# Kernel optimization log

Hardware: AMD Instinct MI355X
Metric: run time of the kernel (lower is better)

The kernel has to match this reference:

```python
import jax, jax.numpy as jnp
import numpy as np

NH, HD = 8, 32  # num_heads, head_dim (visual_dim=256)
BASE = 10000.0

def _inv_freq(dim):
    return 1.0 / (BASE ** (jnp.arange(0, dim, 2, dtype=jnp.float32) / dim))

def rotate_half(x):
    x1, x2 = jnp.split(x, 2, axis=-1)
    return jnp.concatenate([-x2, x1], axis=-1)

def rope3d_freqs(D, H, W, head_dim):
    zd = head_dim // 3; yd = head_dim // 3; xd = head_dim - zd - yd
    fz = jnp.arange(D, dtype=jnp.float32)[:, None] * _inv_freq(zd)  # [D, zd/2]
    fy = jnp.arange(H, dtype=jnp.float32)[:, None] * _inv_freq(yd)
    fx = jnp.arange(W, dtype=jnp.float32)[:, None] * _inv_freq(xd)
    ez = jnp.broadcast_to(jnp.concatenate([fz, fz], -1)[:, None, None, :], (D, H, W, zd))
    ey = jnp.broadcast_to(jnp.concatenate([fy, fy], -1)[None, :, None, :], (D, H, W, yd))
    ex = jnp.broadcast_to(jnp.concatenate([fx, fx], -1)[None, None, :, :], (D, H, W, xd))
    return jnp.concatenate([ez, ey, ex], axis=-1)  # [D,H,W,head_dim]

def apply_rope(q, freqs):
    return q * jnp.cos(freqs) + rotate_half(q) * jnp.sin(freqs)

def setup_inputs() -> dict:
    key = jax.random.key(0)
    ks = jax.random.split(key, 16)
    B, C, D, H, W, S, TD = 2, 256, 32, 32, 32, 256, 512
    s = 0.02
    return {
        'fused_visual': jax.random.normal(ks[0], (B, C, D, H, W), jnp.float32),
        'text_embedding': jax.random.normal(ks[1], (B, S, TD), jnp.float32),
        'q_w': jax.random.normal(ks[2], (C, C), jnp.float32) * s,
        'q_b': jnp.zeros((C,), jnp.float32),
        'k_w': jax.random.normal(ks[3], (TD, C), jnp.float32) * s,
        'k_b': jnp.zeros((C,), jnp.float32),
        'v_w': jax.random.normal(ks[4], (TD, C), jnp.float32) * s,
        'v_b': jnp.zeros((C,), jnp.float32),
        'o_w': jax.random.normal(ks[5], (C, C), jnp.float32) * s,
        'o_b': jnp.zeros((C,), jnp.float32),
        'm1_w': jax.random.normal(ks[6], (TD, TD // 2), jnp.float32) * s,
        'm1_b': jnp.zeros((TD // 2,), jnp.float32),
        'm2_w': jax.random.normal(ks[7], (TD // 2, NH * HD), jnp.float32) * s,
        'm2_b': jnp.zeros((NH * HD,), jnp.float32),
    }

def reference(fused_visual, text_embedding, q_w, q_b, k_w, k_b, v_w, v_b,
              o_w, o_b, m1_w, m1_b, m2_w, m2_b):
    B, C, D, H, W = fused_visual.shape
    S = text_embedding.shape[1]
    scale = HD ** -0.5
    fv = jnp.transpose(fused_visual, (0, 2, 3, 4, 1))  # [B,D,H,W,C]
    q = (fv @ q_w + q_b).reshape(B, D, H, W, NH, HD)
    q = jnp.transpose(q, (0, 4, 1, 2, 3, 5))            # [B,nH,D,H,W,hd]
    k = jnp.transpose((text_embedding @ k_w + k_b).reshape(B, S, NH, HD), (0, 2, 1, 3))
    v = jnp.transpose((text_embedding @ v_w + v_b).reshape(B, S, NH, HD), (0, 2, 1, 3))
    freqs = rope3d_freqs(D, H, W, HD)[None, None]       # [1,1,D,H,W,hd]
    q_rot = apply_rope(q, freqs)
    # learned text phase (exact GELU as in torch default)
    h = jax.nn.gelu(text_embedding @ m1_w + m1_b, approximate=False)
    phase = jnp.transpose((h @ m2_w + m2_b).reshape(B, S, NH, HD), (0, 2, 1, 3))
    k_rot = apply_rope(k, phase)
    q_flat = q_rot.reshape(B, NH, D * H * W, HD)
    attn = jax.nn.softmax(jnp.einsum('bhnd,bhsd->bhns', q_flat, k_rot) * scale, axis=-1)
    out = jnp.einsum('bhns,bhsd->bhnd', attn, v)        # [B,nH,N,hd]
    out = out.reshape(B, NH, D, H, W, HD)
    out = jnp.transpose(out, (0, 2, 3, 4, 1, 5)).reshape(B, D, H, W, C)
    out = out @ o_w + o_b
    return jnp.transpose(out, (0, 4, 1, 2, 3))          # [B,C,D,H,W]
```

## Files before the change

### kernel.cpp

```cpp
#include <hip/hip_runtime.h>
#include <hip/hip_bf16.h>

#define NHD 8
#define HD  32
#define C_  256
#define TD_ 512
#define S_  256
#define N_  32768
#define B_  2

typedef short bf16x8 __attribute__((ext_vector_type(8)));
typedef short bf16x4 __attribute__((ext_vector_type(4)));
typedef float f32x4  __attribute__((ext_vector_type(4)));

#define MFMA16(a,b,c) __builtin_amdgcn_mfma_f32_16x16x32_bf16(a,b,c,0,0,0)

__device__ __forceinline__ short f2bf(float f){
    __hip_bfloat16 h = __float2bfloat16(f);
    return *reinterpret_cast<short*>(&h);
}

typedef __attribute__((address_space(3))) unsigned int lds_u32;
typedef const __attribute__((address_space(1))) unsigned int glb_u32;

__device__ __forceinline__ void async_cp16(const void* g, void* l){
    __builtin_amdgcn_global_load_lds(
        (glb_u32*)(unsigned long long)g,
        (lds_u32*)(unsigned int)(unsigned long long)l,
        16, 0, 0);
}

__device__ __forceinline__ void stage_tile(const short* __restrict__ g, short* l, int tid){
    const int wvb = tid & 192;
#pragma unroll
    for (int r = 0; r < 4; ++r)
        async_cp16(g + (r * 256 + tid) * 8, l + (r * 256 + wvb) * 8);
}

#define TS_LD(Ka, Va, Ma, Ta, j0) \
    _Pragma("unroll") for (int i = 0; i < 16; ++i) { \
        Ka[i] = kp[(j0 + i) * C_]; Va[i] = vp[(j0 + i) * C_]; \
        Ma[i] = mp[(j0 + i) * C_]; Ta[i] = t_s[(j0) + i]; }
#define TS_FM(Ka, Va, Ma, Ta) \
    _Pragma("unroll") for (int i = 0; i < 16; ++i) { \
        kv += Ta[i] * Ka[i]; vv += Ta[i] * Va[i]; hv += Ta[i] * Ma[i]; }
#define M2_LD(Ha, Ga, j0) \
    _Pragma("unroll") for (int i = 0; i < 16; ++i) { \
        Ha[i] = h_s[(j0) + i]; Ga[i] = m2p[(j0 + i) * C_]; }
#define M2_FM(Ha, Ga) \
    _Pragma("unroll") for (int i = 0; i < 16; ++i) { ph += Ha[i] * Ga[i]; }

__global__ __launch_bounds__(256, 2) void text_stage(
    const float* __restrict__ text,
    const float* __restrict__ k_w, const float* __restrict__ k_b,
    const float* __restrict__ v_w, const float* __restrict__ v_b,
    const float* __restrict__ m1_w, const float* __restrict__ m1_b,
    const float* __restrict__ m2_w, const float* __restrict__ m2_b,
    const float* __restrict__ qw, const float* __restrict__ ow,
    short* __restrict__ kf, short* __restrict__ vf,
    short* __restrict__ wqf, short* __restrict__ wof)
{
    const int tid = threadIdx.x;

    if (blockIdx.x >= 512) {
        int gid = (blockIdx.x - 512) * 256 + tid;
        int m = gid >> 13;
        int rest = gid & 8191;
        const float* src = m ? ow : qw;
        short* dst = m ? wof : wqf;
        int lane = rest & 63;
        int l15 = lane & 15, qd = lane >> 4;
        int cbase, co;
        if (m == 0) { int nt = rest >> 9, cc = (rest >> 6) & 7; cbase = cc * 32 + qd * 8; co = nt * 16 + l15; }
        else        { int hm = rest >> 6; cbase = (hm >> 4) * 32 + qd * 8; co = (hm & 15) * 16 + l15; }
        bf16x8 r;
#pragma unroll
        for (int j = 0; j < 8; ++j) r[j] = f2bf(src[(size_t)(cbase + j) * 256 + co]);
        *(bf16x8*)&dst[(size_t)rest * 8] = r;
        return;
    }

    __shared__ float t_s[TD_];
    __shared__ float h_s[C_];
    __shared__ float k_s[C_];
    const int token = blockIdx.x;

    float2 tt = *(const float2*)&text[(size_t)token * TD_ + tid * 2];
    t_s[tid * 2] = tt.x; t_s[tid * 2 + 1] = tt.y;
    __syncthreads();

    float kv = k_b[tid], vv = v_b[tid], hv = m1_b[tid];
    const float* kp = k_w + tid;
    const float* vp = v_w + tid;
    const float* mp = m1_w + tid;

    {
        float Ka[16], Va[16], Ma[16], Ta[16];
        float Kb[16], Vb[16], Mb[16], Tb[16];
        TS_LD(Ka, Va, Ma, Ta, 0);
#pragma unroll 1
        for (int jb = 0; jb < TD_; jb += 32) {
            TS_LD(Kb, Vb, Mb, Tb, jb + 16);
            TS_FM(Ka, Va, Ma, Ta);
            if (jb + 32 < TD_) { TS_LD(Ka, Va, Ma, Ta, jb + 32); }
            TS_FM(Kb, Vb, Mb, Tb);
        }
    }

    float hg = 0.5f * hv * (1.0f + erff(hv * 0.70710678118654752f));
    h_s[tid] = hg;
    k_s[tid] = kv;
    __syncthreads();

    float ph = m2_b[tid];
    const float* m2p = m2_w + tid;
    {
        float Ha[16], Ga[16], Hb[16], Gb[16];
        M2_LD(Ha, Ga, 0);
#pragma unroll 1
        for (int jb = 0; jb < C_; jb += 32) {
            M2_LD(Hb, Gb, jb + 16);
            M2_FM(Ha, Ga);
            if (jb + 32 < C_) { M2_LD(Ha, Ga, jb + 32); }
            M2_FM(Hb, Gb);
        }
    }

    const int t = tid & (HD - 1);
    const int nh = tid >> 5;
    const int b = token >> 8, s = token & (S_ - 1);
    const int bh = b * NHD + nh;
    float partner = (t < 16) ? -k_s[tid + 16] : k_s[tid - 16];
    float kr = kv * cosf(ph) + partner * sinf(ph);
    kf[(((size_t)bh * 16 + (s >> 4)) * 64 + (t >> 3) * 16 + (s & 15)) * 8 + (t & 7)] = f2bf(kr);
    vf[((((size_t)bh * 8 + (s >> 5)) * 2 + (t >> 4)) * 64 + ((s >> 3) & 3) * 16 + (t & 15)) * 8 + (s & 7)] = f2bf(vv);
}

__device__ __forceinline__ float freq3d(int t, int n){
    int d = n >> 10, h = (n >> 5) & 31, w = n & 31;
    float pos, ex;
    if (t < 10)      { pos = (float)d; ex = (float)(2 * (t % 5)) * 0.1f; }
    else if (t < 20) { pos = (float)h; ex = (float)(2 * ((t - 10) % 5)) * 0.1f; }
    else             { pos = (float)w; ex = (float)(2 * ((t - 20) % 6)) * (1.0f / 12.0f); }
    return pos * expf(-ex * 9.210340371976184f);
}

__global__ __launch_bounds__(256, 4) void fused_visual(
    const float* __restrict__ fv, const short* __restrict__ wqf,
    const float* __restrict__ q_b, const short* __restrict__ kf,
    const short* __restrict__ vf, const short* __restrict__ wof,
    const float* __restrict__ o_b, float* __restrict__ out)
{
    __shared__ __align__(16) short Stg[16384];
    __shared__ __align__(16) short Pb[4 * 16 * 64];
    const int tid = threadIdx.x;
    const int lane = tid & 63;
    const int l15 = tid & 15, qd = (tid >> 4) & 3, wv = tid >> 6;
    const int n0 = blockIdx.x * 64;
    const int b = blockIdx.y;
    const f32x4 z4 = {0.f, 0.f, 0.f, 0.f};
    const float scale = 0.17677669529663687f;

    short* slot0 = Stg;
    short* slot1 = Stg + 8192;

    bf16x8 af[8];
    const float* Tsf = (const float*)Stg;
#pragma unroll
    for (int ch = 0; ch < 2; ++ch) {
#pragma unroll
        for (int r = 0; r < 8; ++r) {
            int slot = r * 256 + tid;
            int c_loc = slot >> 4;
            int u = (slot & 15) ^ (c_loc & 15);
            async_cp16(fv + (size_t)(b * C_ + ch * 128 + c_loc) * N_ + n0 + u * 4,
                       Stg + (r * 256 + (tid & 192)) * 8);
        }
        __syncthreads();
#pragma unroll
        for (int cc2 = 0; cc2 < 4; ++cc2) {
            bf16x8 a;
#pragma unroll
            for (int j = 0; j < 8; ++j) {
                int c_loc = cc2 * 32 + qd * 8 + j;
                int u = (wv * 4 + (l15 >> 2)) ^ (c_loc & 15);
                float x = Tsf[c_loc * 64 + u * 4 + (l15 & 3)];
                a[j] = f2bf(x);
            }
            af[ch * 4 + cc2] = a;
        }
        __syncthreads();
    }

    f32x4 acc[16];
#pragma unroll
    for (int i = 0; i < 16; ++i) acc[i] = z4;

    stage_tile(wqf, slot0, tid);

#pragma unroll
    for (int ntp = 0; ntp < 8; ++ntp) {
        __syncthreads();
        if (ntp < 7) stage_tile(wqf + (ntp + 1) * 8192, (ntp & 1) ? slot0 : slot1, tid);
        const short* sb = (ntp & 1) ? slot1 : slot0;
#pragma unroll
        for (int cc = 0; cc < 8; ++cc)
#pragma unroll
            for (int ntl = 0; ntl < 2; ++ntl) {
                bf16x8 bq = *(const bf16x8*)&sb[((ntl * 8 + cc) * 64 + lane) * 8];
                acc[ntp * 2 + ntl] = MFMA16(af[cc], bq, acc[ntp * 2 + ntl]);
            }
    }
    __syncthreads();

    short* Qsc = Stg + wv * 4096;
#pragma unroll
    for (int r = 0; r < 4; ++r) {
        int lr = qd * 4 + r;
        int n = n0 + wv * 16 + lr;
        int key = lr & 7;
        float f1 = freq3d(l15, n), f2 = freq3d(l15 + 16, n);
        float c1 = cosf(f1), s1 = sinf(f1), c2 = cosf(f2), s2 = sinf(f2);
#pragma unroll
        for (int hh = 0; hh < 8; ++hh) {
            float x1 = acc[2 * hh][r]     + q_b[hh * 32 + l15];
            float x2 = acc[2 * hh + 1][r] + q_b[hh * 32 + 16 + l15];
            int cb1 = (hh * 4 + (l15 >> 3)) ^ key;
            int cb2 = (hh * 4 + 2 + (l15 >> 3)) ^ key;
            Qsc[lr * 256 + cb1 * 8 + (l15 & 7)] = f2bf((x1 * c1 - x2 * s1) * scale);
            Qsc[lr * 256 + cb2 * 8 + (l15 & 7)] = f2bf((x2 * c2 + x1 * s2) * scale);
        }
    }
    bf16x8 aqh[8];
#pragma unroll
    for (int h = 0; h < 8; ++h)
        aqh[h] = *(const bf16x8*)&Qsc[l15 * 256 + ((h * 4 + qd) ^ (l15 & 7)) * 8];

    __syncthreads();
    stage_tile(kf + (size_t)(b * NHD) * 8192, slot0, tid);

    f32x4 acc_co[16];
#pragma unroll
    for (int i = 0; i < 16; ++i) acc_co[i] = z4;
    short* Pw = Pb + wv * 16 * 64;
    short* Ow = Pw;

#pragma unroll
    for (int h = 0; h < 8; ++h) {
        const int bh = b * NHD + h;
        __syncthreads();
        stage_tile(wof + (size_t)h * 8192, slot1, tid);

        const short* vbase = vf + (size_t)bh * 8192;

        float tsum[4] = {0.f, 0.f, 0.f, 0.f};
        f32x4 o0 = z4, o1 = z4;

#pragma unroll
        for (int qt = 0; qt < 4; ++qt) {
            f32x4 sc[4];
#pragma unroll
            for (int s4 = 0; s4 < 4; ++s4) {
                bf16x8 bk = *(const bf16x8*)&slot0[(qt * 4 + s4) * 512 + lane * 8];
                sc[s4] = MFMA16(aqh[h], bk, z4);
            }
#pragma unroll
            for (int s4 = 0; s4 < 4; ++s4)
#pragma unroll
                for (int r = 0; r < 4; ++r) {
                    sc[s4][r] = __expf(sc[s4][r]);
                    tsum[r] += sc[s4][r];
                }
#pragma unroll
            for (int s4 = 0; s4 < 4; ++s4)
#pragma unroll
                for (int r = 0; r < 4; ++r) {
                    int row = qd * 4 + r;
                    Pw[row * 64 + ((s4 * 2 + (l15 >> 3)) ^ (row & 7)) * 8 + (l15 & 7)] = f2bf(sc[s4][r]);
                }
#pragma unroll
            for (int ktl = 0; ktl < 2; ++ktl) {
                bf16x8 pa = *(const bf16x8*)&Pw[l15 * 64 + ((ktl * 4 + qd) ^ (l15 & 7)) * 8];
                int kt = qt * 2 + ktl;
                bf16x8 v0 = *(const bf16x8*)&vbase[(kt * 2 + 0) * 512 + lane * 8];
                bf16x8 v1 = *(const bf16x8*)&vbase[(kt * 2 + 1) * 512 + lane * 8];
                o0 = MFMA16(pa, v0, o0);
                o1 = MFMA16(pa, v1, o1);
            }
        }
        float il[4];
#pragma unroll
        for (int r = 0; r < 4; ++r) {
            float t = tsum[r];
            t += __shfl_xor(t, 1); t += __shfl_xor(t, 2);
            t += __shfl_xor(t, 4); t += __shfl_xor(t, 8);
            il[r] = 1.f / t;
        }
#pragma unroll
        for (int r = 0; r < 4; ++r) {
            int row = qd * 4 + r;
            int key = row & 3;
            Ow[row * 32 + (((l15 >> 3) ^ key) & 3) * 8 + (l15 & 7)]       = f2bf(o0[r] * il[r]);
            Ow[row * 32 + (((2 + (l15 >> 3)) ^ key) & 3) * 8 + (l15 & 7)] = f2bf(o1[r] * il[r]);
        }

        __syncthreads();
        if (h < 7)
            stage_tile(kf + (size_t)(bh + 1) * 8192, slot0, tid);

        bf16x8 bo = *(const bf16x8*)&Ow[l15 * 32 + ((qd ^ (l15 & 3)) & 3) * 8];
#pragma unroll
        for (int mt = 0; mt < 16; ++mt) {
            bf16x8 ao = *(const bf16x8*)&slot1[mt * 512 + lane * 8];
            acc_co[mt] = MFMA16(ao, bo, acc_co[mt]);
        }
    }

#pragma unroll
    for (int mt = 0; mt < 16; ++mt)
#pragma unroll
        for (int r = 0; r < 4; ++r) {
            int co = mt * 16 + qd * 4 + r;
            out[(size_t)(b * C_ + co) * N_ + n0 + wv * 16 + l15] = acc_co[mt][r] + o_b[co];
        }
}

extern "C" void kernel_launch(void* const* d_in, const int* in_sizes, int n_in,
                              void* d_out, int out_size, void* d_ws, size_t ws_size,
                              hipStream_t stream) {
    (void)in_sizes; (void)n_in; (void)out_size; (void)ws_size;
    const float* fv   = (const float*)d_in[0];
    const float* text = (const float*)d_in[1];
    const float* q_w  = (const float*)d_in[2];
    const float* q_b  = (const float*)d_in[3];
    const float* k_w  = (const float*)d_in[4];
    const float* k_b  = (const float*)d_in[5];
    const float* v_w  = (const float*)d_in[6];
    const float* v_b  = (const float*)d_in[7];
    const float* o_w  = (const float*)d_in[8];
    const float* o_b  = (const float*)d_in[9];
    const float* m1_w = (const float*)d_in[10];
    const float* m1_b = (const float*)d_in[11];
    const float* m2_w = (const float*)d_in[12];
    const float* m2_b = (const float*)d_in[13];
    float* out = (float*)d_out;

    short* wsS  = (short*)d_ws;
    short* kf   = wsS;
    short* vf   = wsS + 131072;
    short* wqf  = wsS + 262144;
    short* wof  = wsS + 327680;

    hipLaunchKernelGGL(text_stage, dim3(576), dim3(256), 0, stream,
                       text, k_w, k_b, v_w, v_b, m1_w, m1_b, m2_w, m2_b,
                       q_w, o_w, kf, vf, wqf, wof);
    hipLaunchKernelGGL(fused_visual, dim3(512, 2), dim3(256), 0, stream,
                       fv, wqf, q_b, kf, vf, wof, o_b, out);
}
```

Baseline: 270.0 us.

## Split text stage into two batched-token kernels and load visual input directly

The per-token text projection kernel becomes two kernels. text1 handles 4 tokens per block for the K/V/M1 projections plus GELU, and text2 handles 8 tokens per block for the M2 phase projection and the K RoPE. Weight loads are reused across several tokens, which cuts redundant global weight traffic, at the cost of an extra launch and fp32 intermediates round-tripping through the workspace. In the visual kernel, the input tile is now read directly from global memory into registers instead of staged through LDS, and the first Wq tile stage is issued earlier so it overlaps that load.

```diff
diff --git a/kernel.cpp b/kernel.cpp
--- a/kernel.cpp
+++ b/kernel.cpp
@@ -37,33 +37,25 @@
         async_cp16(g + (r * 256 + tid) * 8, l + (r * 256 + wvb) * 8);
 }
 
-#define TS_LD(Ka, Va, Ma, Ta, j0) \
-    _Pragma("unroll") for (int i = 0; i < 16; ++i) { \
-        Ka[i] = kp[(j0 + i) * C_]; Va[i] = vp[(j0 + i) * C_]; \
-        Ma[i] = mp[(j0 + i) * C_]; Ta[i] = t_s[(j0) + i]; }
-#define TS_FM(Ka, Va, Ma, Ta) \
-    _Pragma("unroll") for (int i = 0; i < 16; ++i) { \
-        kv += Ta[i] * Ka[i]; vv += Ta[i] * Va[i]; hv += Ta[i] * Ma[i]; }
-#define M2_LD(Ha, Ga, j0) \
-    _Pragma("unroll") for (int i = 0; i < 16; ++i) { \
-        Ha[i] = h_s[(j0) + i]; Ga[i] = m2p[(j0 + i) * C_]; }
-#define M2_FM(Ha, Ga) \
-    _Pragma("unroll") for (int i = 0; i < 16; ++i) { ph += Ha[i] * Ga[i]; }
-
-__global__ __launch_bounds__(256, 2) void text_stage(
+#define T1_LD(K,V,M,j0) _Pragma("unroll") for(int i=0;i<8;++i){ \
+    K[i]=kp[(j0+i)*C_]; V[i]=vp[(j0+i)*C_]; M[i]=mp[(j0+i)*C_]; }
+#define T1_FM(K,V,M,j0) _Pragma("unroll") for(int i=0;i<8;++i){ \
+    _Pragma("unroll") for(int m=0;m<4;++m){ float tv=t_s[m*TD_+j0+i]; \
+        accK[m]+=tv*K[i]; accV[m]+=tv*V[i]; accH[m]+=tv*M[i]; } }
+
+__global__ __launch_bounds__(256) void text1(
     const float* __restrict__ text,
     const float* __restrict__ k_w, const float* __restrict__ k_b,
     const float* __restrict__ v_w, const float* __restrict__ v_b,
     const float* __restrict__ m1_w, const float* __restrict__ m1_b,
-    const float* __restrict__ m2_w, const float* __restrict__ m2_b,
     const float* __restrict__ qw, const float* __restrict__ ow,
-    short* __restrict__ kf, short* __restrict__ vf,
+    float* __restrict__ kraw, float* __restrict__ vraw, float* __restrict__ hgb,
     short* __restrict__ wqf, short* __restrict__ wof)
 {
     const int tid = threadIdx.x;
 
-    if (blockIdx.x >= 512) {
-        int gid = (blockIdx.x - 512) * 256 + tid;
+    if (blockIdx.x >= 128) {
+        int gid = (blockIdx.x - 128) * 256 + tid;
         int m = gid >> 13;
         int rest = gid & 8191;
         const float* src = m ? ow : qw;
@@ -80,60 +72,95 @@
         return;
     }
 
-    __shared__ float t_s[TD_];
-    __shared__ float h_s[C_];
-    __shared__ float k_s[C_];
-    const int token = blockIdx.x;
-
-    float2 tt = *(const float2*)&text[(size_t)token * TD_ + tid * 2];
-    t_s[tid * 2] = tt.x; t_s[tid * 2 + 1] = tt.y;
+    __shared__ float t_s[4 * TD_];
+    const int tok0 = blockIdx.x * 4;
+#pragma unroll
+    for (int i = 0; i < 2; ++i) {
+        int idx = i * 256 + tid;
+        *(float4*)&t_s[idx * 4] = *(const float4*)&text[(size_t)tok0 * TD_ + idx * 4];
+    }
     __syncthreads();
 
-    float kv = k_b[tid], vv = v_b[tid], hv = m1_b[tid];
+    float accK[4], accV[4], accH[4];
+#pragma unroll
+    for (int m = 0; m < 4; ++m) { accK[m] = k_b[tid]; accV[m] = v_b[tid]; accH[m] = m1_b[tid]; }
     const float* kp = k_w + tid;
     const float* vp = v_w + tid;
     const float* mp = m1_w + tid;
 
     {
-        float Ka[16], Va[16], Ma[16], Ta[16];
-        float Kb[16], Vb[16], Mb[16], Tb[16];
-        TS_LD(Ka, Va, Ma, Ta, 0);
+        float ka[8], va[8], ma[8], kb2[8], vb2[8], mb2[8];
+        T1_LD(ka, va, ma, 0);
 #pragma unroll 1
-        for (int jb = 0; jb < TD_; jb += 32) {
-            TS_LD(Kb, Vb, Mb, Tb, jb + 16);
-            TS_FM(Ka, Va, Ma, Ta);
-            if (jb + 32 < TD_) { TS_LD(Ka, Va, Ma, Ta, jb + 32); }
-            TS_FM(Kb, Vb, Mb, Tb);
-        }
-    }
-
-    float hg = 0.5f * hv * (1.0f + erff(hv * 0.70710678118654752f));
-    h_s[tid] = hg;
-    k_s[tid] = kv;
+        for (int j0 = 0; j0 < TD_; j0 += 16) {
+            T1_LD(kb2, vb2, mb2, j0 + 8);
+            T1_FM(ka, va, ma, j0);
+            if (j0 + 16 < TD_) { T1_LD(ka, va, ma, j0 + 16); }
+            T1_FM(kb2, vb2, mb2, j0 + 8);
+        }
+    }
+
+#pragma unroll
+    for (int m = 0; m < 4; ++m) {
+        kraw[(size_t)(tok0 + m) * C_ + tid] = accK[m];
+        vraw[(size_t)(tok0 + m) * C_ + tid] = accV[m];
+        float hv = accH[m];
+        hgb[(size_t)(tok0 + m) * C_ + tid] = 0.5f * hv * (1.0f + erff(hv * 0.70710678118654752f));
+    }
+}
+
+#define T2_LD(G, j0) _Pragma("unroll") for (int i = 0; i < 8; ++i) G[i] = m2p[(j0 + i) * C_];
+#define T2_FM(G, j0) _Pragma("unroll") for (int i = 0; i < 8; ++i) { \
+    _Pragma("unroll") for (int m = 0; m < 8; ++m) accP[m] += h_s[m * C_ + j0 + i] * G[i]; }
+
+__global__ __launch_bounds__(256) void text2(
+    const float* __restrict__ m2_w, const float* __restrict__ m2_b,
+    const float* __restrict__ kraw, const float* __restrict__ vraw,
+    const float* __restrict__ hgb,
+    short* __restrict__ kf, short* __restrict__ vf)
+{
+    __shared__ float h_s[8 * C_];
+    const int tid = threadIdx.x;
+    const int tok0 = blockIdx.x * 8;
+#pragma unroll
+    for (int i = 0; i < 2; ++i) {
+        int idx = i * 256 + tid;
+        *(float4*)&h_s[idx * 4] = *(const float4*)&hgb[(size_t)tok0 * C_ + idx * 4];
+    }
     __syncthreads();
 
-    float ph = m2_b[tid];
+    float accP[8];
+#pragma unroll
+    for (int m = 0; m < 8; ++m) accP[m] = m2_b[tid];
     const float* m2p = m2_w + tid;
     {
-        float Ha[16], Ga[16], Hb[16], Gb[16];
-        M2_LD(Ha, Ga, 0);
+        float ga[8], gb2[8];
+        T2_LD(ga, 0);
 #pragma unroll 1
-        for (int jb = 0; jb < C_; jb += 32) {
-            M2_LD(Hb, Gb, jb + 16);
-            M2_FM(Ha, Ga);
-            if (jb + 32 < C_) { M2_LD(Ha, Ga, jb + 32); }
-            M2_FM(Hb, Gb);
+        for (int j0 = 0; j0 < C_; j0 += 16) {
+            T2_LD(gb2, j0 + 8);
+            T2_FM(ga, j0);
+            if (j0 + 16 < C_) { T2_LD(ga, j0 + 16); }
+            T2_FM(gb2, j0 + 8);
         }
     }
 
     const int t = tid & (HD - 1);
     const int nh = tid >> 5;
-    const int b = token >> 8, s = token & (S_ - 1);
-    const int bh = b * NHD + nh;
-    float partner = (t < 16) ? -k_s[tid + 16] : k_s[tid - 16];
-    float kr = kv * cosf(ph) + partner * sinf(ph);
-    kf[(((size_t)bh * 16 + (s >> 4)) * 64 + (t >> 3) * 16 + (s & 15)) * 8 + (t & 7)] = f2bf(kr);
-    vf[((((size_t)bh * 8 + (s >> 5)) * 2 + (t >> 4)) * 64 + ((s >> 3) & 3) * 16 + (t & 15)) * 8 + (s & 7)] = f2bf(vv);
+#pragma unroll
+    for (int m = 0; m < 8; ++m) {
+        int token = tok0 + m;
+        int b = token >> 8, s = token & (S_ - 1);
+        int bh = b * NHD + nh;
+        float kv = kraw[(size_t)token * C_ + tid];
+        float vv = vraw[(size_t)token * C_ + tid];
+        float partner = (t < 16) ? -kraw[(size_t)token * C_ + tid + 16]
+                                 :  kraw[(size_t)token * C_ + tid - 16];
+        float ph = accP[m];
+        float kr = kv * cosf(ph) + partner * sinf(ph);
+        kf[(((size_t)bh * 16 + (s >> 4)) * 64 + (t >> 3) * 16 + (s & 15)) * 8 + (t & 7)] = f2bf(kr);
+        vf[((((size_t)bh * 8 + (s >> 5)) * 2 + (t >> 4)) * 64 + ((s >> 3) & 3) * 16 + (t & 15)) * 8 + (s & 7)] = f2bf(vv);
+    }
 }
 
 __device__ __forceinline__ float freq3d(int t, int n){
@@ -164,39 +191,25 @@
     short* slot0 = Stg;
     short* slot1 = Stg + 8192;
 
+    stage_tile(wqf, slot0, tid);
+
     bf16x8 af[8];
-    const float* Tsf = (const float*)Stg;
-#pragma unroll
-    for (int ch = 0; ch < 2; ++ch) {
-#pragma unroll
-        for (int r = 0; r < 8; ++r) {
-            int slot = r * 256 + tid;
-            int c_loc = slot >> 4;
-            int u = (slot & 15) ^ (c_loc & 15);
-            async_cp16(fv + (size_t)(b * C_ + ch * 128 + c_loc) * N_ + n0 + u * 4,
-                       Stg + (r * 256 + (tid & 192)) * 8);
-        }
-        __syncthreads();
-#pragma unroll
-        for (int cc2 = 0; cc2 < 4; ++cc2) {
-            bf16x8 a;
-#pragma unroll
-            for (int j = 0; j < 8; ++j) {
-                int c_loc = cc2 * 32 + qd * 8 + j;
-                int u = (wv * 4 + (l15 >> 2)) ^ (c_loc & 15);
-                float x = Tsf[c_loc * 64 + u * 4 + (l15 & 3)];
-                a[j] = f2bf(x);
-            }
-            af[ch * 4 + cc2] = a;
-        }
-        __syncthreads();
+    {
+        const float* fbase = fv + ((size_t)b * C_) * N_ + n0 + wv * 16 + l15;
+#pragma unroll
+        for (int cc = 0; cc < 8; ++cc) {
+            float tmp[8];
+#pragma unroll
+            for (int j = 0; j < 8; ++j)
+                tmp[j] = fbase[(size_t)(cc * 32 + qd * 8 + j) * N_];
+#pragma unroll
+            for (int j = 0; j < 8; ++j) af[cc][j] = f2bf(tmp[j]);
+        }
     }
 
     f32x4 acc[16];
 #pragma unroll
     for (int i = 0; i < 16; ++i) acc[i] = z4;
-
-    stage_tile(wqf, slot0, tid);
 
 #pragma unroll
     for (int ntp = 0; ntp < 8; ++ntp) {
@@ -350,10 +363,15 @@
     short* vf   = wsS + 131072;
     short* wqf  = wsS + 262144;
     short* wof  = wsS + 327680;
-
-    hipLaunchKernelGGL(text_stage, dim3(576), dim3(256), 0, stream,
-                       text, k_w, k_b, v_w, v_b, m1_w, m1_b, m2_w, m2_b,
-                       q_w, o_w, kf, vf, wqf, wof);
+    float* kraw = (float*)(wsS + 393216);
+    float* vraw = kraw + 131072;
+    float* hgb  = kraw + 262144;
+
+    hipLaunchKernelGGL(text1, dim3(192), dim3(256), 0, stream,
+                       text, k_w, k_b, v_w, v_b, m1_w, m1_b,
+                       q_w, o_w, kraw, vraw, hgb, wqf, wof);
+    hipLaunchKernelGGL(text2, dim3(64), dim3(256), 0, stream,
+                       m2_w, m2_b, kraw, vraw, hgb, kf, vf);
     hipLaunchKernelGGL(fused_visual, dim3(512, 2), dim3(256), 0, stream,
                        fv, wqf, q_b, kf, vf, wof, o_b, out);
 }
```

New measurement: 309.0 us. 14.4% more time.
